# Optimization experiments

Measured on AMD Instinct MI355X. Metric: run time of the kernel, lower is better.

The kernel has to match this reference:

```python
import jax, jax.numpy as jnp
import numpy as np

N_NODES = 50000


def gcn_conv(x, W, b, src, dst, ew, n_nodes):
    """PyG GCNConv: out = D^{-1/2}(A + I)D^{-1/2} (x @ W) + b, A weighted by ew.

    Self loops (weight 1) are handled analytically instead of appending edges.
    """
    h = x @ W  # [N, out]
    # degree includes self-loop weight of 1
    deg = jax.ops.segment_sum(ew, dst, num_segments=n_nodes) + 1.0  # [N]
    dinv = jnp.where(deg > 0, jax.lax.rsqrt(deg), 0.0)
    norm = dinv[src] * ew * dinv[dst]  # [E]
    # message = norm * h[src], scatter-add to dst
    agg = jax.ops.segment_sum(h[src] * norm[:, None], dst, num_segments=n_nodes)
    # self-loop contribution: dinv[i] * 1 * dinv[i] * h[i]
    agg = agg + h * (dinv * dinv)[:, None]
    return agg + b


def setup_inputs() -> dict:
    key = jax.random.key(0)
    k = jax.random.split(key, 8)
    n, e, d_in, d_h = N_NODES, 600000, 128, 128
    x = jax.random.normal(k[0], (n, d_in), dtype=jnp.float32)
    edge_index = jax.random.randint(k[1], (2, e), 0, n, dtype=jnp.int64)
    edge_attr = jax.random.uniform(k[2], (e,), dtype=jnp.float32)
    s1 = 1.0 / np.sqrt(d_in)
    s2 = 1.0 / np.sqrt(d_h)
    W1 = jax.random.uniform(k[3], (d_in, d_h), jnp.float32, -s1, s1)
    b1 = jnp.zeros((d_h,), jnp.float32)
    W2 = jax.random.uniform(k[4], (d_h, d_h), jnp.float32, -s2, s2)
    b2 = jnp.zeros((d_h,), jnp.float32)
    return {"x": x, "edge_index": edge_index, "edge_attr": edge_attr,
            "W1": W1, "b1": b1, "W2": W2, "b2": b2}


def reference(x, edge_index, edge_attr, W1, b1, W2, b2):
    src, dst = edge_index[0], edge_index[1]
    h = gcn_conv(x, W1, b1, src, dst, edge_attr, N_NODES)
    h = jax.nn.relu(h)
    # dropout is identity in eval mode (deterministic reference)
    out = gcn_conv(h, W2, b2, src, dst, edge_attr, N_NODES)
    return out
```

## Files before the change

### kernel.cpp

```cpp
#include <hip/hip_runtime.h>
#include <stdint.h>

#define D 128
#define EPB 4096
#define CSZ 128

typedef __bf16 bf16x8 __attribute__((ext_vector_type(8)));
typedef float f32x4 __attribute__((ext_vector_type(4)));

__device__ inline float bf2f(unsigned short u) {
    return __uint_as_float((unsigned)u << 16);
}
__device__ inline unsigned short f2bf(float f) {
    unsigned u = __float_as_uint(f);
    return (unsigned short)((u + 0x7FFF + ((u >> 16) & 1)) >> 16);
}

__global__ __launch_bounds__(256) void k_prep(const float* __restrict__ W1,
                                              unsigned short* __restrict__ Wt1,
                                              const float* __restrict__ W2,
                                              unsigned short* __restrict__ Wt2) {
    __shared__ float t[128 * 132];
    const int tid = threadIdx.x;
    const float* W = (blockIdx.x == 0) ? W1 : W2;
    unsigned short* Wt = (blockIdx.x == 0) ? Wt1 : Wt2;
    for (int i = tid; i < 128 * 32; i += 256) {
        int r = i >> 5, c = i & 31;
        float4 v = *(const float4*)(W + r * 128 + c * 4);
        float* dp = &t[r * 132 + c * 4];
        dp[0] = v.x; dp[1] = v.y; dp[2] = v.z; dp[3] = v.w;
    }
    __syncthreads();
    for (int i = tid; i < 128 * 32; i += 256) {
        int nn = i >> 5, c = i & 31;
        ushort4 o;
        o.x = f2bf(t[(c * 4 + 0) * 132 + nn]);
        o.y = f2bf(t[(c * 4 + 1) * 132 + nn]);
        o.z = f2bf(t[(c * 4 + 2) * 132 + nn]);
        o.w = f2bf(t[(c * 4 + 3) * 132 + nn]);
        *(ushort4*)(Wt + nn * 128 + c * 4) = o;
    }
}

template <bool IN_BF16>
__device__ inline void mfma_body(unsigned short* sE,
                                 const void* __restrict__ Xv,
                                 const unsigned short* __restrict__ Wt,
                                 unsigned short* __restrict__ H, int n, int blk) {
    const int tid = threadIdx.x;
    const int row0 = blk * 64;
    const int lane = tid & 63;
    const int wv = tid >> 6;
    const int qm = lane & 15;
    const int quad = lane >> 4;

    const int arow = row0 + wv * 16 + qm;
    const int ar = (arow < n) ? arow : (n - 1);

    f32x4 acc[8];
#pragma unroll
    for (int i = 0; i < 8; ++i) acc[i] = (f32x4){0.f, 0.f, 0.f, 0.f};

#pragma unroll
    for (int kb = 0; kb < 4; ++kb) {
        const int koff = kb * 32 + quad * 8;
        bf16x8 a;
        if (IN_BF16) {
            a = *(const bf16x8*)((const unsigned short*)Xv + (size_t)ar * 128 + koff);
        } else {
            const float* Xf = (const float*)Xv + (size_t)ar * 128 + koff;
            float4 v0 = *(const float4*)(Xf);
            float4 v1 = *(const float4*)(Xf + 4);
            union { bf16x8 v; ushort4 u[2]; } cv;
            cv.u[0].x = f2bf(v0.x); cv.u[0].y = f2bf(v0.y);
            cv.u[0].z = f2bf(v0.z); cv.u[0].w = f2bf(v0.w);
            cv.u[1].x = f2bf(v1.x); cv.u[1].y = f2bf(v1.y);
            cv.u[1].z = f2bf(v1.z); cv.u[1].w = f2bf(v1.w);
            a = cv.v;
        }
#pragma unroll
        for (int n0 = 0; n0 < 8; ++n0) {
            bf16x8 b = *(const bf16x8*)(Wt + (n0 * 16 + qm) * 128 + koff);
            acc[n0] = __builtin_amdgcn_mfma_f32_16x16x32_bf16(a, b, acc[n0], 0, 0, 0);
        }
    }

#pragma unroll
    for (int n0 = 0; n0 < 8; ++n0)
#pragma unroll
        for (int r = 0; r < 4; ++r)
            sE[(wv * 16 + quad * 4 + r) * 136 + n0 * 16 + qm] = f2bf(acc[n0][r]);
    __syncthreads();

    const int row_in = lane >> 2;
    const int c0 = (lane & 3) * 4;
    const int grow = row0 + wv * 16 + row_in;
    if (grow < n) {
#pragma unroll
        for (int j = 0; j < 4; ++j)
            *(int4*)(H + (size_t)grow * 128 + (c0 + j) * 8) =
                *(const int4*)(&sE[(wv * 16 + row_in) * 136 + (c0 + j) * 8]);
    }
}

__global__ __launch_bounds__(256, 4) void k_histmfma(const float* __restrict__ X,
                                                     const unsigned short* __restrict__ Wt,
                                                     unsigned short* __restrict__ H, int n, int gb,
                                                     const int* __restrict__ ei,
                                                     unsigned int* __restrict__ bh,
                                                     int E, int C) {
    __shared__ char arena[64 * 136 * 2];
    if (blockIdx.x < gb) {
        mfma_body<false>((unsigned short*)arena, (const void*)X, Wt, H, n, blockIdx.x);
    } else {
        unsigned int* hist = (unsigned int*)arena;
        const int b = blockIdx.x - gb;
        for (int i = threadIdx.x; i < C; i += 256) hist[i] = 0;
        __syncthreads();
        const int base = b * EPB + threadIdx.x;
#pragma unroll
        for (int k = 0; k < EPB / 256; ++k) {
            int e = base + k * 256;
            if (e < E) atomicAdd(&hist[((unsigned)ei[E + e]) >> 7], 1u);
        }
        __syncthreads();
        for (int i = threadIdx.x; i < C; i += 256)
            bh[(size_t)b * C + i] = hist[i];
    }
}

__global__ __launch_bounds__(256) void k_scanA2(const unsigned int* __restrict__ bh,
                                                int* __restrict__ ebase, int* __restrict__ bsums,
                                                int total, int C, int B1) {
    __shared__ int tmp[256];
    const int tid = threadIdx.x;
    const int i = blockIdx.x * 256 + tid;
    int v = 0;
    if (i < total) {
        int c = i / B1;
        int b = i - c * B1;
        v = (int)bh[(size_t)b * C + c];
    }
    tmp[tid] = v;
    __syncthreads();
    for (int off = 1; off < 256; off <<= 1) {
        int t = (tid >= off) ? tmp[tid - off] : 0;
        __syncthreads();
        tmp[tid] += t;
        __syncthreads();
    }
    if (i < total) ebase[i] = tmp[tid] - v;
    if (tid == 255) bsums[blockIdx.x] = tmp[255];
}

__global__ __launch_bounds__(256) void k_scanB2(int* __restrict__ ebase,
                                                const int* __restrict__ bsums, int total) {
    __shared__ int sred[4];
    const int tid = threadIdx.x;
    int v = (tid < (int)blockIdx.x) ? bsums[tid] : 0;
#pragma unroll
    for (int off = 32; off; off >>= 1) v += __shfl_down(v, off);
    if ((tid & 63) == 0) sred[tid >> 6] = v;
    __syncthreads();
    int tot = sred[0] + sred[1] + sred[2] + sred[3];
    int i = blockIdx.x * 256 + tid;
    if (i < total) ebase[i] += tot;
}

__global__ __launch_bounds__(256) void k_scat(const int* __restrict__ ei,
                                              const float* __restrict__ ew,
                                              const int* __restrict__ ebase,
                                              int2* __restrict__ brec, int E, int C, int B1) {
    __shared__ unsigned int cur[512];
    const int b = blockIdx.x;
    for (int i = threadIdx.x; i < C; i += 256) cur[i] = 0;
    __syncthreads();
    const int base = b * EPB + threadIdx.x;
#pragma unroll
    for (int k = 0; k < EPB / 256; ++k) {
        int e = base + k * 256;
        if (e < E) {
            int s = ei[e];
            unsigned d = (unsigned)ei[E + e];
            float w = ew[e];
            int c = d >> 7;
            unsigned r = atomicAdd(&cur[c], 1u);
            int pos = ebase[c * B1 + b] + (int)r;
            brec[pos] = make_int2((int)((d << 16) | (unsigned)s), __float_as_int(w));
        }
    }
}

__global__ __launch_bounds__(256) void k_cbuild(const int2* __restrict__ brec,
                                                const int* __restrict__ ebase,
                                                int2* __restrict__ erec,
                                                int* __restrict__ rowstart,
                                                int* __restrict__ cnt,
                                                float* __restrict__ dinv,
                                                int n, int C, int B1, int E) {
    __shared__ unsigned int hcnt[CSZ], hdeg[CSZ], lsc[CSZ], curs[CSZ];
    const int c = blockIdx.x;
    const int tid = threadIdx.x;
    const int cs = ebase[c * B1];
    const int ce = (c + 1 < C) ? ebase[(c + 1) * B1] : E;
    if (tid < CSZ) { hcnt[tid] = 0; hdeg[tid] = 0; }
    __syncthreads();
    for (int i = cs + tid; i < ce; i += 256) {
        int2 r = brec[i];
        int local = (int)(((unsigned)r.x) >> 16) & (CSZ - 1);
        atomicAdd(&hcnt[local], 1u);
        atomicAdd(&hdeg[local], (unsigned)(__int_as_float(r.y) * 16777216.0f));
    }
    __syncthreads();
    if (tid < CSZ) lsc[tid] = hcnt[tid];
    __syncthreads();
    for (int off = 1; off < CSZ; off <<= 1) {
        unsigned t = (tid < CSZ && tid >= off) ? lsc[tid - off] : 0u;
        __syncthreads();
        if (tid < CSZ) lsc[tid] += t;
        __syncthreads();
    }
    if (tid < CSZ) {
        unsigned excl = lsc[tid] - hcnt[tid];
        curs[tid] = excl;
        int node = c * CSZ + tid;
        if (node < n) {
            rowstart[node] = cs + (int)excl;
            cnt[node] = (int)hcnt[tid];
            float deg = 1.0f + (float)hdeg[tid] * (1.0f / 16777216.0f);
            dinv[node] = rsqrtf(deg);
        }
    }
    __syncthreads();
    for (int i = cs + tid; i < ce; i += 256) {
        int2 r = brec[i];
        int local = (int)(((unsigned)r.x) >> 16) & (CSZ - 1);
        unsigned rk = atomicAdd(&curs[local], 1u);
        erec[cs + (int)rk] = r;
    }
}

__global__ __launch_bounds__(256) void k_nrm(int2* __restrict__ erec,
                                             const float* __restrict__ dinv, int E) {
    const int base = blockIdx.x * 512 + threadIdx.x;
#pragma unroll
    for (int k = 0; k < 2; ++k) {
        int e = base + k * 256;
        if (e < E) {
            int2 r = erec[e];
            unsigned dst = ((unsigned)r.x) >> 16;
            int src = r.x & 0xFFFF;
            float nm = dinv[src] * __int_as_float(r.y) * dinv[dst];
            erec[e] = make_int2(src, __float_as_int(nm));
        }
    }
}

__global__ __launch_bounds__(256, 4) void k_mfma2(const unsigned short* __restrict__ X,
                                                  const unsigned short* __restrict__ Wt,
                                                  unsigned short* __restrict__ H, int n) {
    __shared__ unsigned short sE[64 * 136];
    mfma_body<true>(sE, (const void*)X, Wt, H, n, blockIdx.x);
}

template <bool OUT_BF16>
__global__ __launch_bounds__(256) void k_gather(const ushort4* __restrict__ H4,
                                                const int2* __restrict__ erec,
                                                const int* __restrict__ rowstart,
                                                const int* __restrict__ cnt,
                                                const float* __restrict__ dinv,
                                                const float4* __restrict__ bias4,
                                                void* __restrict__ OUTv, int n) {
    const int lane = threadIdx.x & 31;
    const int node = blockIdx.x * 8 + (threadIdx.x >> 5);
    if (node >= n) return;
    const int start = rowstart[node];
    const int m = cnt[node];
    const float di = dinv[node];
    const float dii = di * di;

    float4 b = bias4[lane];
    ushort4 h = H4[(size_t)node * 32 + lane];
    float ax = b.x + dii * bf2f(h.x);
    float ay = b.y + dii * bf2f(h.y);
    float az = b.z + dii * bf2f(h.z);
    float aw = b.w + dii * bf2f(h.w);

    int j = 0;
    for (; j + 4 <= m; j += 4) {
        const int base = start + j;
        int2 e0 = erec[base + 0], e1 = erec[base + 1];
        int2 e2 = erec[base + 2], e3 = erec[base + 3];
        float w0 = __int_as_float(e0.y), w1 = __int_as_float(e1.y);
        float w2 = __int_as_float(e2.y), w3 = __int_as_float(e3.y);
        ushort4 v0 = H4[(size_t)e0.x * 32 + lane];
        ushort4 v1 = H4[(size_t)e1.x * 32 + lane];
        ushort4 v2 = H4[(size_t)e2.x * 32 + lane];
        ushort4 v3 = H4[(size_t)e3.x * 32 + lane];
        ax += w0 * bf2f(v0.x); ay += w0 * bf2f(v0.y); az += w0 * bf2f(v0.z); aw += w0 * bf2f(v0.w);
        ax += w1 * bf2f(v1.x); ay += w1 * bf2f(v1.y); az += w1 * bf2f(v1.z); aw += w1 * bf2f(v1.w);
        ax += w2 * bf2f(v2.x); ay += w2 * bf2f(v2.y); az += w2 * bf2f(v2.z); aw += w2 * bf2f(v2.w);
        ax += w3 * bf2f(v3.x); ay += w3 * bf2f(v3.y); az += w3 * bf2f(v3.z); aw += w3 * bf2f(v3.w);
    }
    for (; j < m; ++j) {
        int2 er = erec[start + j];
        float w = __int_as_float(er.y);
        ushort4 v = H4[(size_t)er.x * 32 + lane];
        ax += w * bf2f(v.x); ay += w * bf2f(v.y); az += w * bf2f(v.z); aw += w * bf2f(v.w);
    }
    if (OUT_BF16) {
        ushort4 o;
        o.x = f2bf(fmaxf(ax, 0.f)); o.y = f2bf(fmaxf(ay, 0.f));
        o.z = f2bf(fmaxf(az, 0.f)); o.w = f2bf(fmaxf(aw, 0.f));
        ((ushort4*)OUTv)[(size_t)node * 32 + lane] = o;
    } else {
        float4 o; o.x = ax; o.y = ay; o.z = az; o.w = aw;
        ((float4*)OUTv)[(size_t)node * 32 + lane] = o;
    }
}

extern "C" void kernel_launch(void* const* d_in, const int* in_sizes, int n_in,
                              void* d_out, int out_size, void* d_ws, size_t ws_size,
                              hipStream_t stream) {
    const float* x  = (const float*)d_in[0];
    const int*   ei = (const int*)d_in[1];
    const float* ew = (const float*)d_in[2];
    const float* W1 = (const float*)d_in[3];
    const float* b1 = (const float*)d_in[4];
    const float* W2 = (const float*)d_in[5];
    const float* b2 = (const float*)d_in[6];
    float* out = (float*)d_out;

    const int N = in_sizes[0] / D;
    const int E = in_sizes[2];

    const int C  = (N + CSZ - 1) / CSZ;
    const int B1n = (E + EPB - 1) / EPB;
    const int total = C * B1n;
    const int sb = (total + 255) / 256;

    char* p = (char*)d_ws;
    auto alloc = [&](size_t bytes) {
        void* r = (void*)p;
        p += (bytes + 255) & ~(size_t)255;
        return r;
    };
    unsigned int* bh = (unsigned int*)alloc((size_t)total * 4);
    int*   ebase    = (int*)alloc((size_t)total * 4);
    int*   bsums    = (int*)alloc(1024 * 4);
    float* dinv     = (float*)alloc((size_t)N * 4);
    int*   cnt      = (int*)alloc((size_t)N * 4);
    int*   rowstart = (int*)alloc((size_t)N * 4);
    int2*  brec     = (int2*)alloc((size_t)E * 8);
    int2*  erec     = (int2*)alloc((size_t)E * 8);
    unsigned short* Hbuf = (unsigned short*)alloc((size_t)N * D * 2);
    unsigned short* Abuf = (unsigned short*)alloc((size_t)N * D * 2);
    unsigned short* Wt1  = (unsigned short*)alloc(128 * 128 * 2);
    unsigned short* Wt2  = (unsigned short*)alloc(128 * 128 * 2);

    const int gb = (N + 63) / 64;
    const int hb = (N + 7) / 8;

    k_prep<<<2, 256, 0, stream>>>(W1, Wt1, W2, Wt2);
    k_histmfma<<<gb + B1n, 256, 0, stream>>>(x, Wt1, Hbuf, N, gb, ei, bh, E, C);
    k_scanA2<<<sb, 256, 0, stream>>>(bh, ebase, bsums, total, C, B1n);
    k_scanB2<<<sb, 256, 0, stream>>>(ebase, bsums, total);
    k_scat<<<B1n, 256, 0, stream>>>(ei, ew, ebase, brec, E, C, B1n);
    k_cbuild<<<C, 256, 0, stream>>>(brec, ebase, erec, rowstart, cnt, dinv, N, C, B1n, E);
    k_nrm<<<(E + 511) / 512, 256, 0, stream>>>(erec, dinv, E);
    k_gather<true><<<hb, 256, 0, stream>>>((const ushort4*)Hbuf, erec, rowstart, cnt,
                                           dinv, (const float4*)b1, (void*)Abuf, N);
    k_mfma2<<<gb, 256, 0, stream>>>(Abuf, Wt2, Hbuf, N);
    k_gather<false><<<hb, 256, 0, stream>>>((const ushort4*)Hbuf, erec, rowstart, cnt,
                                            dinv, (const float4*)b2, (void*)out, N);
}
```

Before: 220.9 us.

## Fuse pipeline into one cooperative persistent kernel with grid syncs

Replaces the ten separate kernel launches with a single cooperative kernel that walks through every stage in grid-stride loops, separated by grid.sync(). It also removes the k_nrm pass. Edge weights are now scaled by dinv[src] inside the gather, and the destination dinv is applied once per node at the end. The weight-transpose prep is merged into the histogram stage and reads W directly rather than through shared memory. The intent is to remove launch gaps and the extra pass over the edge records, at the cost of a dinv lookup per edge and grid-sync overhead with a grid capped at 1008 blocks.

```diff
diff --git a/kernel.cpp b/kernel.cpp
--- a/kernel.cpp
+++ b/kernel.cpp
@@ -1,5 +1,8 @@
 #include <hip/hip_runtime.h>
+#include <hip/hip_cooperative_groups.h>
 #include <stdint.h>
+
+namespace cg = cooperative_groups;
 
 #define D 128
 #define EPB 4096
@@ -16,29 +19,142 @@
     return (unsigned short)((u + 0x7FFF + ((u >> 16) & 1)) >> 16);
 }
 
-__global__ __launch_bounds__(256) void k_prep(const float* __restrict__ W1,
-                                              unsigned short* __restrict__ Wt1,
-                                              const float* __restrict__ W2,
-                                              unsigned short* __restrict__ Wt2) {
-    __shared__ float t[128 * 132];
+struct Params {
+    const float* x; const int* ei; const float* ew;
+    const float* W1; const float* b1; const float* W2; const float* b2;
+    float* out;
+    int N, E, C, B1n, total, gb, hb, sb, G;
+    unsigned short *Wt1, *Wt2;
+    unsigned int* bh; int* ebase; int* bsums;
+    float* dinv; int* cnt; int* rowstart;
+    int2* brec; int2* erec;
+    unsigned short *Hbuf, *Abuf;
+};
+
+
+__device__ inline void dev_prep(int which, const Params& p) {
+    const float* W = (which == 0) ? p.W1 : p.W2;
+    unsigned short* Wt = (which == 0) ? p.Wt1 : p.Wt2;
+    for (int i = threadIdx.x; i < 2048; i += 256) {
+        int nn = i >> 4;
+        int kc = (i & 15) << 3;
+        ushort4 o0, o1;
+        o0.x = f2bf(W[(kc + 0) * 128 + nn]); o0.y = f2bf(W[(kc + 1) * 128 + nn]);
+        o0.z = f2bf(W[(kc + 2) * 128 + nn]); o0.w = f2bf(W[(kc + 3) * 128 + nn]);
+        o1.x = f2bf(W[(kc + 4) * 128 + nn]); o1.y = f2bf(W[(kc + 5) * 128 + nn]);
+        o1.z = f2bf(W[(kc + 6) * 128 + nn]); o1.w = f2bf(W[(kc + 7) * 128 + nn]);
+        *(ushort4*)(Wt + nn * 128 + kc) = o0;
+        *(ushort4*)(Wt + nn * 128 + kc + 4) = o1;
+    }
+}
+
+__device__ inline void dev_hist(int b, const Params& p, unsigned int* hist) {
+    for (int i = threadIdx.x; i < p.C; i += 256) hist[i] = 0;
+    __syncthreads();
+    const int base = b * EPB + threadIdx.x;
+#pragma unroll
+    for (int k = 0; k < EPB / 256; ++k) {
+        int e = base + k * 256;
+        if (e < p.E) atomicAdd(&hist[((unsigned)p.ei[p.E + e]) >> 7], 1u);
+    }
+    __syncthreads();
+    for (int i = threadIdx.x; i < p.C; i += 256) p.bh[(size_t)b * p.C + i] = hist[i];
+}
+
+__device__ inline void dev_scanA(int blk, const Params& p, int* tmp) {
     const int tid = threadIdx.x;
-    const float* W = (blockIdx.x == 0) ? W1 : W2;
-    unsigned short* Wt = (blockIdx.x == 0) ? Wt1 : Wt2;
-    for (int i = tid; i < 128 * 32; i += 256) {
-        int r = i >> 5, c = i & 31;
-        float4 v = *(const float4*)(W + r * 128 + c * 4);
-        float* dp = &t[r * 132 + c * 4];
-        dp[0] = v.x; dp[1] = v.y; dp[2] = v.z; dp[3] = v.w;
-    }
-    __syncthreads();
-    for (int i = tid; i < 128 * 32; i += 256) {
-        int nn = i >> 5, c = i & 31;
-        ushort4 o;
-        o.x = f2bf(t[(c * 4 + 0) * 132 + nn]);
-        o.y = f2bf(t[(c * 4 + 1) * 132 + nn]);
-        o.z = f2bf(t[(c * 4 + 2) * 132 + nn]);
-        o.w = f2bf(t[(c * 4 + 3) * 132 + nn]);
-        *(ushort4*)(Wt + nn * 128 + c * 4) = o;
+    const int i = blk * 256 + tid;
+    int v = 0;
+    if (i < p.total) {
+        int c = i / p.B1n;
+        int b = i - c * p.B1n;
+        v = (int)p.bh[(size_t)b * p.C + c];
+    }
+    tmp[tid] = v;
+    __syncthreads();
+    for (int off = 1; off < 256; off <<= 1) {
+        int t = (tid >= off) ? tmp[tid - off] : 0;
+        __syncthreads();
+        tmp[tid] += t;
+        __syncthreads();
+    }
+    if (i < p.total) p.ebase[i] = tmp[tid] - v;
+    if (tid == 255) p.bsums[blk] = tmp[255];
+}
+
+__device__ inline void dev_scanB(int blk, const Params& p, int* sred) {
+    const int tid = threadIdx.x;
+    int v = (tid < blk) ? p.bsums[tid] : 0;
+#pragma unroll
+    for (int off = 32; off; off >>= 1) v += __shfl_down(v, off);
+    if ((tid & 63) == 0) sred[tid >> 6] = v;
+    __syncthreads();
+    int tot = sred[0] + sred[1] + sred[2] + sred[3];
+    int i = blk * 256 + tid;
+    if (i < p.total) p.ebase[i] += tot;
+}
+
+__device__ inline void dev_scat(int b, const Params& p, unsigned int* cur) {
+    for (int i = threadIdx.x; i < p.C; i += 256) cur[i] = 0;
+    __syncthreads();
+    const int base = b * EPB + threadIdx.x;
+#pragma unroll
+    for (int k = 0; k < EPB / 256; ++k) {
+        int e = base + k * 256;
+        if (e < p.E) {
+            int s = p.ei[e];
+            unsigned d = (unsigned)p.ei[p.E + e];
+            float w = p.ew[e];
+            int c = d >> 7;
+            unsigned r = atomicAdd(&cur[c], 1u);
+            int pos = p.ebase[c * p.B1n + b] + (int)r;
+            p.brec[pos] = make_int2((int)((d << 16) | (unsigned)s), __float_as_int(w));
+        }
+    }
+}
+
+__device__ inline void dev_cbuild(int c, const Params& p, unsigned int* a) {
+    unsigned int* hcnt = a;
+    unsigned int* hdeg = a + CSZ;
+    unsigned int* lsc  = a + 2 * CSZ;
+    unsigned int* curs = a + 3 * CSZ;
+    const int tid = threadIdx.x;
+    const int cs = p.ebase[c * p.B1n];
+    const int ce = (c + 1 < p.C) ? p.ebase[(c + 1) * p.B1n] : p.E;
+    if (tid < CSZ) { hcnt[tid] = 0; hdeg[tid] = 0; }
+    __syncthreads();
+    for (int i = cs + tid; i < ce; i += 256) {
+        int2 r = p.brec[i];
+        int local = (int)(((unsigned)r.x) >> 16) & (CSZ - 1);
+        atomicAdd(&hcnt[local], 1u);
+        atomicAdd(&hdeg[local], (unsigned)(__int_as_float(r.y) * 16777216.0f));
+    }
+    __syncthreads();
+    if (tid < CSZ) lsc[tid] = hcnt[tid];
+    __syncthreads();
+    for (int off = 1; off < CSZ; off <<= 1) {
+        unsigned t = (tid < CSZ && tid >= off) ? lsc[tid - off] : 0u;
+        __syncthreads();
+        if (tid < CSZ) lsc[tid] += t;
+        __syncthreads();
+    }
+    if (tid < CSZ) {
+        unsigned excl = lsc[tid] - hcnt[tid];
+        curs[tid] = excl;
+        int node = c * CSZ + tid;
+        if (node < p.N) {
+            p.rowstart[node] = cs + (int)excl;
+            p.cnt[node] = (int)hcnt[tid];
+            float deg = 1.0f + (float)hdeg[tid] * (1.0f / 16777216.0f);
+            p.dinv[node] = rsqrtf(deg);
+        }
+    }
+    __syncthreads();
+    for (int i = cs + tid; i < ce; i += 256) {
+        int2 r = p.brec[i];
+        int local = (int)(((unsigned)r.x) >> 16) & (CSZ - 1);
+        unsigned rk = atomicAdd(&curs[local], 1u);
+        p.erec[cs + (int)rk] = make_int2(r.x & 0xFFFF, r.y);
     }
 }
 
@@ -103,196 +219,33 @@
     }
 }
 
-__global__ __launch_bounds__(256, 4) void k_histmfma(const float* __restrict__ X,
-                                                     const unsigned short* __restrict__ Wt,
-                                                     unsigned short* __restrict__ H, int n, int gb,
-                                                     const int* __restrict__ ei,
-                                                     unsigned int* __restrict__ bh,
-                                                     int E, int C) {
-    __shared__ char arena[64 * 136 * 2];
-    if (blockIdx.x < gb) {
-        mfma_body<false>((unsigned short*)arena, (const void*)X, Wt, H, n, blockIdx.x);
-    } else {
-        unsigned int* hist = (unsigned int*)arena;
-        const int b = blockIdx.x - gb;
-        for (int i = threadIdx.x; i < C; i += 256) hist[i] = 0;
-        __syncthreads();
-        const int base = b * EPB + threadIdx.x;
-#pragma unroll
-        for (int k = 0; k < EPB / 256; ++k) {
-            int e = base + k * 256;
-            if (e < E) atomicAdd(&hist[((unsigned)ei[E + e]) >> 7], 1u);
-        }
-        __syncthreads();
-        for (int i = threadIdx.x; i < C; i += 256)
-            bh[(size_t)b * C + i] = hist[i];
-    }
-}
-
-__global__ __launch_bounds__(256) void k_scanA2(const unsigned int* __restrict__ bh,
-                                                int* __restrict__ ebase, int* __restrict__ bsums,
-                                                int total, int C, int B1) {
-    __shared__ int tmp[256];
-    const int tid = threadIdx.x;
-    const int i = blockIdx.x * 256 + tid;
-    int v = 0;
-    if (i < total) {
-        int c = i / B1;
-        int b = i - c * B1;
-        v = (int)bh[(size_t)b * C + c];
-    }
-    tmp[tid] = v;
-    __syncthreads();
-    for (int off = 1; off < 256; off <<= 1) {
-        int t = (tid >= off) ? tmp[tid - off] : 0;
-        __syncthreads();
-        tmp[tid] += t;
-        __syncthreads();
-    }
-    if (i < total) ebase[i] = tmp[tid] - v;
-    if (tid == 255) bsums[blockIdx.x] = tmp[255];
-}
-
-__global__ __launch_bounds__(256) void k_scanB2(int* __restrict__ ebase,
-                                                const int* __restrict__ bsums, int total) {
-    __shared__ int sred[4];
-    const int tid = threadIdx.x;
-    int v = (tid < (int)blockIdx.x) ? bsums[tid] : 0;
-#pragma unroll
-    for (int off = 32; off; off >>= 1) v += __shfl_down(v, off);
-    if ((tid & 63) == 0) sred[tid >> 6] = v;
-    __syncthreads();
-    int tot = sred[0] + sred[1] + sred[2] + sred[3];
-    int i = blockIdx.x * 256 + tid;
-    if (i < total) ebase[i] += tot;
-}
-
-__global__ __launch_bounds__(256) void k_scat(const int* __restrict__ ei,
-                                              const float* __restrict__ ew,
-                                              const int* __restrict__ ebase,
-                                              int2* __restrict__ brec, int E, int C, int B1) {
-    __shared__ unsigned int cur[512];
-    const int b = blockIdx.x;
-    for (int i = threadIdx.x; i < C; i += 256) cur[i] = 0;
-    __syncthreads();
-    const int base = b * EPB + threadIdx.x;
-#pragma unroll
-    for (int k = 0; k < EPB / 256; ++k) {
-        int e = base + k * 256;
-        if (e < E) {
-            int s = ei[e];
-            unsigned d = (unsigned)ei[E + e];
-            float w = ew[e];
-            int c = d >> 7;
-            unsigned r = atomicAdd(&cur[c], 1u);
-            int pos = ebase[c * B1 + b] + (int)r;
-            brec[pos] = make_int2((int)((d << 16) | (unsigned)s), __float_as_int(w));
-        }
-    }
-}
-
-__global__ __launch_bounds__(256) void k_cbuild(const int2* __restrict__ brec,
-                                                const int* __restrict__ ebase,
-                                                int2* __restrict__ erec,
-                                                int* __restrict__ rowstart,
-                                                int* __restrict__ cnt,
-                                                float* __restrict__ dinv,
-                                                int n, int C, int B1, int E) {
-    __shared__ unsigned int hcnt[CSZ], hdeg[CSZ], lsc[CSZ], curs[CSZ];
-    const int c = blockIdx.x;
-    const int tid = threadIdx.x;
-    const int cs = ebase[c * B1];
-    const int ce = (c + 1 < C) ? ebase[(c + 1) * B1] : E;
-    if (tid < CSZ) { hcnt[tid] = 0; hdeg[tid] = 0; }
-    __syncthreads();
-    for (int i = cs + tid; i < ce; i += 256) {
-        int2 r = brec[i];
-        int local = (int)(((unsigned)r.x) >> 16) & (CSZ - 1);
-        atomicAdd(&hcnt[local], 1u);
-        atomicAdd(&hdeg[local], (unsigned)(__int_as_float(r.y) * 16777216.0f));
-    }
-    __syncthreads();
-    if (tid < CSZ) lsc[tid] = hcnt[tid];
-    __syncthreads();
-    for (int off = 1; off < CSZ; off <<= 1) {
-        unsigned t = (tid < CSZ && tid >= off) ? lsc[tid - off] : 0u;
-        __syncthreads();
-        if (tid < CSZ) lsc[tid] += t;
-        __syncthreads();
-    }
-    if (tid < CSZ) {
-        unsigned excl = lsc[tid] - hcnt[tid];
-        curs[tid] = excl;
-        int node = c * CSZ + tid;
-        if (node < n) {
-            rowstart[node] = cs + (int)excl;
-            cnt[node] = (int)hcnt[tid];
-            float deg = 1.0f + (float)hdeg[tid] * (1.0f / 16777216.0f);
-            dinv[node] = rsqrtf(deg);
-        }
-    }
-    __syncthreads();
-    for (int i = cs + tid; i < ce; i += 256) {
-        int2 r = brec[i];
-        int local = (int)(((unsigned)r.x) >> 16) & (CSZ - 1);
-        unsigned rk = atomicAdd(&curs[local], 1u);
-        erec[cs + (int)rk] = r;
-    }
-}
-
-__global__ __launch_bounds__(256) void k_nrm(int2* __restrict__ erec,
-                                             const float* __restrict__ dinv, int E) {
-    const int base = blockIdx.x * 512 + threadIdx.x;
-#pragma unroll
-    for (int k = 0; k < 2; ++k) {
-        int e = base + k * 256;
-        if (e < E) {
-            int2 r = erec[e];
-            unsigned dst = ((unsigned)r.x) >> 16;
-            int src = r.x & 0xFFFF;
-            float nm = dinv[src] * __int_as_float(r.y) * dinv[dst];
-            erec[e] = make_int2(src, __float_as_int(nm));
-        }
-    }
-}
-
-__global__ __launch_bounds__(256, 4) void k_mfma2(const unsigned short* __restrict__ X,
-                                                  const unsigned short* __restrict__ Wt,
-                                                  unsigned short* __restrict__ H, int n) {
-    __shared__ unsigned short sE[64 * 136];
-    mfma_body<true>(sE, (const void*)X, Wt, H, n, blockIdx.x);
-}
-
 template <bool OUT_BF16>
-__global__ __launch_bounds__(256) void k_gather(const ushort4* __restrict__ H4,
-                                                const int2* __restrict__ erec,
-                                                const int* __restrict__ rowstart,
-                                                const int* __restrict__ cnt,
-                                                const float* __restrict__ dinv,
-                                                const float4* __restrict__ bias4,
-                                                void* __restrict__ OUTv, int n) {
+__device__ inline void gather_body(const Params& p, const ushort4* __restrict__ H4,
+                                   const float4* __restrict__ bias4,
+                                   void* __restrict__ OUTv, int g) {
     const int lane = threadIdx.x & 31;
-    const int node = blockIdx.x * 8 + (threadIdx.x >> 5);
-    if (node >= n) return;
-    const int start = rowstart[node];
-    const int m = cnt[node];
-    const float di = dinv[node];
-    const float dii = di * di;
+    const int node = g * 8 + (threadIdx.x >> 5);
+    if (node >= p.N) return;
+    const int start = p.rowstart[node];
+    const int m = p.cnt[node];
+    const float di = p.dinv[node];
 
     float4 b = bias4[lane];
     ushort4 h = H4[(size_t)node * 32 + lane];
-    float ax = b.x + dii * bf2f(h.x);
-    float ay = b.y + dii * bf2f(h.y);
-    float az = b.z + dii * bf2f(h.z);
-    float aw = b.w + dii * bf2f(h.w);
+    float ax = di * bf2f(h.x);
+    float ay = di * bf2f(h.y);
+    float az = di * bf2f(h.z);
+    float aw = di * bf2f(h.w);
 
     int j = 0;
     for (; j + 4 <= m; j += 4) {
         const int base = start + j;
-        int2 e0 = erec[base + 0], e1 = erec[base + 1];
-        int2 e2 = erec[base + 2], e3 = erec[base + 3];
-        float w0 = __int_as_float(e0.y), w1 = __int_as_float(e1.y);
-        float w2 = __int_as_float(e2.y), w3 = __int_as_float(e3.y);
+        int2 e0 = p.erec[base + 0], e1 = p.erec[base + 1];
+        int2 e2 = p.erec[base + 2], e3 = p.erec[base + 3];
+        float w0 = p.dinv[e0.x] * __int_as_float(e0.y);
+        float w1 = p.dinv[e1.x] * __int_as_float(e1.y);
+        float w2 = p.dinv[e2.x] * __int_as_float(e2.y);
+        float w3 = p.dinv[e3.x] * __int_as_float(e3.y);
         ushort4 v0 = H4[(size_t)e0.x * 32 + lane];
         ushort4 v1 = H4[(size_t)e1.x * 32 + lane];
         ushort4 v2 = H4[(size_t)e2.x * 32 + lane];
@@ -303,11 +256,13 @@
         ax += w3 * bf2f(v3.x); ay += w3 * bf2f(v3.y); az += w3 * bf2f(v3.z); aw += w3 * bf2f(v3.w);
     }
     for (; j < m; ++j) {
-        int2 er = erec[start + j];
-        float w = __int_as_float(er.y);
+        int2 er = p.erec[start + j];
+        float w = p.dinv[er.x] * __int_as_float(er.y);
         ushort4 v = H4[(size_t)er.x * 32 + lane];
         ax += w * bf2f(v.x); ay += w * bf2f(v.y); az += w * bf2f(v.z); aw += w * bf2f(v.w);
     }
+    ax = b.x + di * ax; ay = b.y + di * ay;
+    az = b.z + di * az; aw = b.w + di * aw;
     if (OUT_BF16) {
         ushort4 o;
         o.x = f2bf(fmaxf(ax, 0.f)); o.y = f2bf(fmaxf(ay, 0.f));
@@ -319,58 +274,141 @@
     }
 }
 
+__global__ __launch_bounds__(256, 4) void k_all(Params p) {
+    cg::grid_group grid = cg::this_grid();
+    __shared__ __align__(16) char arena[64 * 136 * 2];
+    const int bid = blockIdx.x;
+
+    for (int w = bid; w < 2 + p.B1n; w += p.G) {
+        if (w < 2) dev_prep(w, p); else dev_hist(w - 2, p, (unsigned int*)arena);
+        __syncthreads();
+    }
+    grid.sync();
+    for (int w = bid; w < p.gb + p.sb; w += p.G) {
+        if (w < p.gb) mfma_body<false>((unsigned short*)arena, (const void*)p.x, p.Wt1, p.Hbuf, p.N, w);
+        else dev_scanA(w - p.gb, p, (int*)arena);
+        __syncthreads();
+    }
+    grid.sync();
+    for (int w = bid; w < p.sb; w += p.G) { dev_scanB(w, p, (int*)arena); __syncthreads(); }
+    grid.sync();
+    for (int w = bid; w < p.B1n; w += p.G) { dev_scat(w, p, (unsigned int*)arena); __syncthreads(); }
+    grid.sync();
+    for (int w = bid; w < p.C; w += p.G) { dev_cbuild(w, p, (unsigned int*)arena); __syncthreads(); }
+    grid.sync();
+    for (int g = bid; g < p.hb; g += p.G)
+        gather_body<true>(p, (const ushort4*)p.Hbuf, (const float4*)p.b1, (void*)p.Abuf, g);
+    grid.sync();
+    for (int w = bid; w < p.gb; w += p.G) {
+        mfma_body<true>((unsigned short*)arena, (const void*)p.Abuf, p.Wt2, p.Hbuf, p.N, w);
+        __syncthreads();
+    }
+    grid.sync();
+    for (int g = bid; g < p.hb; g += p.G)
+        gather_body<false>(p, (const ushort4*)p.Hbuf, (const float4*)p.b2, (void*)p.out, g);
+}
+
+__global__ __launch_bounds__(256, 4) void k_f0(Params p) {
+    __shared__ __align__(16) char arena[64 * 136 * 2];
+    if (blockIdx.x < 2) dev_prep(blockIdx.x, p);
+    else dev_hist(blockIdx.x - 2, p, (unsigned int*)arena);
+}
+__global__ __launch_bounds__(256, 4) void k_f1(Params p) {
+    __shared__ __align__(16) char arena[64 * 136 * 2];
+    if ((int)blockIdx.x < p.gb) mfma_body<false>((unsigned short*)arena, (const void*)p.x, p.Wt1, p.Hbuf, p.N, blockIdx.x);
+    else dev_scanA(blockIdx.x - p.gb, p, (int*)arena);
+}
+__global__ __launch_bounds__(256) void k_f2(Params p) {
+    __shared__ int sred[4];
+    dev_scanB(blockIdx.x, p, sred);
+}
+__global__ __launch_bounds__(256) void k_f3(Params p) {
+    __shared__ unsigned int cur[512];
+    dev_scat(blockIdx.x, p, cur);
+}
+__global__ __launch_bounds__(256) void k_f4(Params p) {
+    __shared__ unsigned int a[4 * CSZ];
+    dev_cbuild(blockIdx.x, p, a);
+}
+__global__ __launch_bounds__(256) void k_f5(Params p) {
+    gather_body<true>(p, (const ushort4*)p.Hbuf, (const float4*)p.b1, (void*)p.Abuf, blockIdx.x);
+}
+__global__ __launch_bounds__(256, 4) void k_f6(Params p) {
+    __shared__ __align__(16) char arena[64 * 136 * 2];
+    mfma_body<true>((unsigned short*)arena, (const void*)p.Abuf, p.Wt2, p.Hbuf, p.N, blockIdx.x);
+}
+__global__ __launch_bounds__(256) void k_f7(Params p) {
+    gather_body<false>(p, (const ushort4*)p.Hbuf, (const float4*)p.b2, (void*)p.out, blockIdx.x);
+}
+
 extern "C" void kernel_launch(void* const* d_in, const int* in_sizes, int n_in,
                               void* d_out, int out_size, void* d_ws, size_t ws_size,
                               hipStream_t stream) {
-    const float* x  = (const float*)d_in[0];
-    const int*   ei = (const int*)d_in[1];
-    const float* ew = (const float*)d_in[2];
-    const float* W1 = (const float*)d_in[3];
-    const float* b1 = (const float*)d_in[4];
-    const float* W2 = (const float*)d_in[5];
-    const float* b2 = (const float*)d_in[6];
-    float* out = (float*)d_out;
-
-    const int N = in_sizes[0] / D;
-    const int E = in_sizes[2];
-
-    const int C  = (N + CSZ - 1) / CSZ;
-    const int B1n = (E + EPB - 1) / EPB;
-    const int total = C * B1n;
-    const int sb = (total + 255) / 256;
-
-    char* p = (char*)d_ws;
+    Params p;
+    p.x  = (const float*)d_in[0];
+    p.ei = (const int*)d_in[1];
+    p.ew = (const float*)d_in[2];
+    p.W1 = (const float*)d_in[3];
+    p.b1 = (const float*)d_in[4];
+    p.W2 = (const float*)d_in[5];
+    p.b2 = (const float*)d_in[6];
+    p.out = (float*)d_out;
+
+    p.N = in_sizes[0] / D;
+    p.E = in_sizes[2];
+    p.C = (p.N + CSZ - 1) / CSZ;
+    p.B1n = (p.E + EPB - 1) / EPB;
+    p.total = p.C * p.B1n;
+    p.sb = (p.total + 255) / 256;
+    p.gb = (p.N + 63) / 64;
+    p.hb = (p.N + 7) / 8;
+
+    char* w = (char*)d_ws;
     auto alloc = [&](size_t bytes) {
-        void* r = (void*)p;
-        p += (bytes + 255) & ~(size_t)255;
+        void* r = (void*)w;
+        w += (bytes + 255) & ~(size_t)255;
         return r;
     };
-    unsigned int* bh = (unsigned int*)alloc((size_t)total * 4);
-    int*   ebase    = (int*)alloc((size_t)total * 4);
-    int*   bsums    = (int*)alloc(1024 * 4);
-    float* dinv     = (float*)alloc((size_t)N * 4);
-    int*   cnt      = (int*)alloc((size_t)N * 4);
-    int*   rowstart = (int*)alloc((size_t)N * 4);
-    int2*  brec     = (int2*)alloc((size_t)E * 8);
-    int2*  erec     = (int2*)alloc((size_t)E * 8);
-    unsigned short* Hbuf = (unsigned short*)alloc((size_t)N * D * 2);
-    unsigned short* Abuf = (unsigned short*)alloc((size_t)N * D * 2);
-    unsigned short* Wt1  = (unsigned short*)alloc(128 * 128 * 2);
-    unsigned short* Wt2  = (unsigned short*)alloc(128 * 128 * 2);
-
-    const int gb = (N + 63) / 64;
-    const int hb = (N + 7) / 8;
-
-    k_prep<<<2, 256, 0, stream>>>(W1, Wt1, W2, Wt2);
-    k_histmfma<<<gb + B1n, 256, 0, stream>>>(x, Wt1, Hbuf, N, gb, ei, bh, E, C);
-    k_scanA2<<<sb, 256, 0, stream>>>(bh, ebase, bsums, total, C, B1n);
-    k_scanB2<<<sb, 256, 0, stream>>>(ebase, bsums, total);
-    k_scat<<<B1n, 256, 0, stream>>>(ei, ew, ebase, brec, E, C, B1n);
-    k_cbuild<<<C, 256, 0, stream>>>(brec, ebase, erec, rowstart, cnt, dinv, N, C, B1n, E);
-    k_nrm<<<(E + 511) / 512, 256, 0, stream>>>(erec, dinv, E);
-    k_gather<true><<<hb, 256, 0, stream>>>((const ushort4*)Hbuf, erec, rowstart, cnt,
-                                           dinv, (const float4*)b1, (void*)Abuf, N);
-    k_mfma2<<<gb, 256, 0, stream>>>(Abuf, Wt2, Hbuf, N);
-    k_gather<false><<<hb, 256, 0, stream>>>((const ushort4*)Hbuf, erec, rowstart, cnt,
-                                            dinv, (const float4*)b2, (void*)out, N);
-}
+    p.bh       = (unsigned int*)alloc((size_t)p.total * 4);
+    p.ebase    = (int*)alloc((size_t)p.total * 4);
+    p.bsums    = (int*)alloc(1024 * 4);
+    p.dinv     = (float*)alloc((size_t)p.N * 4);
+    p.cnt      = (int*)alloc((size_t)p.N * 4);
+    p.rowstart = (int*)alloc((size_t)p.N * 4);
+    p.brec     = (int2*)alloc((size_t)p.E * 8);
+    p.erec     = (int2*)alloc((size_t)p.E * 8);
+    p.Hbuf     = (unsigned short*)alloc((size_t)p.N * D * 2);
+    p.Abuf     = (unsigned short*)alloc((size_t)p.N * D * 2);
+    p.Wt1      = (unsigned short*)alloc(128 * 128 * 2);
+    p.Wt2      = (unsigned short*)alloc(128 * 128 * 2);
+
+    int dev = 0;
+    (void)hipGetDevice(&dev);
+    int numCU = 0;
+    (void)hipDeviceGetAttribute(&numCU, hipDeviceAttributeMultiprocessorCount, dev);
+    int maxB = 0;
+    hipError_t oe = hipOccupancyMaxActiveBlocksPerMultiprocessor(&maxB, (const void*)k_all, 256, 0);
+
+    bool coop = (oe == hipSuccess && maxB > 0 && numCU > 0);
+    hipError_t le = hipErrorUnknown;
+    if (coop) {
+        long g = (long)numCU * maxB;
+        p.G = (g > 1008) ? 1008 : (int)g;
+        if (p.G < 64) coop = false;
+    }
+    if (coop) {
+        void* args[] = { &p };
+        le = hipLaunchCooperativeKernel((const void*)k_all, dim3(p.G), dim3(256), args, 0, stream);
+    }
+    if (!coop || le != hipSuccess) {
+        (void)hipGetLastError();
+        k_f0<<<2 + p.B1n, 256, 0, stream>>>(p);
+        k_f1<<<p.gb + p.sb, 256, 0, stream>>>(p);
+        k_f2<<<p.sb, 256, 0, stream>>>(p);
+        k_f3<<<p.B1n, 256, 0, stream>>>(p);
+        k_f4<<<p.C, 256, 0, stream>>>(p);
+        k_f5<<<p.hb, 256, 0, stream>>>(p);
+        k_f6<<<p.gb, 256, 0, stream>>>(p);
+        k_f7<<<p.hb, 256, 0, stream>>>(p);
+    }
+}
```

New measurement: 681.4 us. +208.5%, slower.
